# Performance work log

Measured on AMD Instinct MI355X. Metric: run time of the kernel, lower is better.

Reference implementation:

```python
import jax, jax.numpy as jnp
import numpy as np
from jax import lax

L, H = 16384, 1024
EPS = 1e-5


def _ln(x, w, b):
    m = jnp.mean(x, axis=-1, keepdims=True)
    v = jnp.var(x, axis=-1, keepdims=True)
    return (x - m) * lax.rsqrt(v + EPS) * w + b


def setup_inputs() -> dict:
    key = jax.random.key(0)
    ks = jax.random.split(key, 12)
    s = 0.02
    return {
        "x": jax.random.normal(ks[0], (L, H), dtype=jnp.float32),
        "ln1_w": jnp.ones((H,), jnp.float32),
        "ln1_b": jnp.zeros((H,), jnp.float32),
        "W_in": jax.random.normal(ks[1], (H, H), jnp.float32) * s,
        "b_in": jnp.zeros((H,), jnp.float32),
        "W_gate": jax.random.normal(ks[2], (H, H), jnp.float32) * s,
        "b_gate": jnp.zeros((H,), jnp.float32),
        "W_out": jax.random.normal(ks[3], (H, H), jnp.float32) * s,
        "b_out": jnp.zeros((H,), jnp.float32),
        "state_decay": jnp.zeros((H,), jnp.float32),
        "ln2_w": jnp.ones((H,), jnp.float32),
        "ln2_b": jnp.zeros((H,), jnp.float32),
        "W_ff1": jax.random.normal(ks[4], (H, 2 * H), jnp.float32) * s,
        "b_ff1": jnp.zeros((2 * H,), jnp.float32),
        "W_ff2": jax.random.normal(ks[5], (2 * H, H), jnp.float32) * s,
        "b_ff2": jnp.zeros((H,), jnp.float32),
    }


def reference(x, ln1_w, ln1_b, W_in, b_in, W_gate, b_gate, W_out, b_out,
              state_decay, ln2_w, ln2_b, W_ff1, b_ff1, W_ff2, b_ff2):
    hidden = _ln(x, ln1_w, ln1_b)                       # [L,H]
    u = hidden @ W_in + b_in                            # [L,H]
    gate = jax.nn.sigmoid(hidden @ W_gate + b_gate)     # [L,H]
    decay = jax.nn.sigmoid(state_decay)                 # [H]

    def step(s, u_t):
        s = decay * s + u_t
        return s, s

    z = jnp.zeros((x.shape[1],), x.dtype)
    _, states_f = lax.scan(step, z, u)                  # forward recurrence
    _, states_b = lax.scan(step, z, u, reverse=True)    # backward recurrence
    state_out = 0.5 * (states_f + states_b) * gate

    x = x + state_out @ W_out + b_out
    h = _ln(x, ln2_w, ln2_b)
    x = x + jax.nn.silu(h @ W_ff1 + b_ff1) @ W_ff2 + b_ff2
    return x
```

## Files before the change

kernel.cpp:

```cpp
#include <hip/hip_runtime.h>
#include <hip/hip_bf16.h>
#include <hip/hip_fp16.h>

#define L_SEQ 16384
#define HDIM  1024
#define CH    32
#define NC    (L_SEQ / CH)

typedef _Float16 f16;
typedef _Float16 f16x8 __attribute__((ext_vector_type(8)));
typedef _Float16 f16x4 __attribute__((ext_vector_type(4)));
typedef float    f32x4 __attribute__((ext_vector_type(4)));

#define AS1(p) (const __attribute__((address_space(1))) void*)(p)
#define AS3(p) (__attribute__((address_space(3))) void*)(p)

__global__ __launch_bounds__(256) void wcvt_t(const float* __restrict__ in,
                                              f16* __restrict__ out, int K, int N) {
  __shared__ float tile[32][33];
  int n0 = blockIdx.x * 32, k0 = blockIdx.y * 32;
  int tx = threadIdx.x, ty = threadIdx.y;
#pragma unroll
  for (int i = 0; i < 4; i++) {
    int k = k0 + ty + i * 8;
    tile[ty + i * 8][tx] = in[(size_t)k * N + n0 + tx];
  }
  __syncthreads();
#pragma unroll
  for (int i = 0; i < 4; i++) {
    int n = n0 + ty + i * 8;
    out[(size_t)n * K + k0 + tx] = (f16)tile[tx][ty + i * 8];
  }
}

__global__ __launch_bounds__(256) void ln_k(const float* __restrict__ x,
                                            const float* __restrict__ w,
                                            const float* __restrict__ b,
                                            f16* __restrict__ out,
                                            f16* __restrict__ xcopy) {
  int row = blockIdx.x;
  int t = threadIdx.x;
  const float4* xr = (const float4*)(x + (size_t)row * HDIM);
  float4 v = xr[t];
  float s  = v.x + v.y + v.z + v.w;
  float s2 = v.x * v.x + v.y * v.y + v.z * v.z + v.w * v.w;
#pragma unroll
  for (int off = 32; off > 0; off >>= 1) {
    s  += __shfl_down(s, off);
    s2 += __shfl_down(s2, off);
  }
  __shared__ float red[8];
  int wid = t >> 6, lane = t & 63;
  if (lane == 0) { red[wid] = s; red[4 + wid] = s2; }
  __syncthreads();
  if (t == 0) {
    red[0] = red[0] + red[1] + red[2] + red[3];
    red[4] = red[4] + red[5] + red[6] + red[7];
  }
  __syncthreads();
  float mean = red[0] * (1.0f / HDIM);
  float var  = red[4] * (1.0f / HDIM) - mean * mean;
  float rstd = rsqrtf(var + 1e-5f);
  float4 ww = ((const float4*)w)[t];
  float4 bb = ((const float4*)b)[t];
  f16x4 o;
  o[0] = (f16)((v.x - mean) * rstd * ww.x + bb.x);
  o[1] = (f16)((v.y - mean) * rstd * ww.y + bb.y);
  o[2] = (f16)((v.z - mean) * rstd * ww.z + bb.z);
  o[3] = (f16)((v.w - mean) * rstd * ww.w + bb.w);
  ((f16x4*)(out + (size_t)row * HDIM))[t] = o;
  if (xcopy) {
    f16x4 c;
    c[0] = (f16)v.x; c[1] = (f16)v.y; c[2] = (f16)v.z; c[3] = (f16)v.w;
    ((f16x4*)(xcopy + (size_t)row * HDIM))[t] = c;
  }
}

__global__ __launch_bounds__(128) void ln_k16(const f16* __restrict__ x,
                                              const float* __restrict__ w,
                                              const float* __restrict__ b,
                                              f16* __restrict__ out) {
  int row = blockIdx.x;
  int t = threadIdx.x;
  f16x8 xv = ((const f16x8*)(x + (size_t)row * HDIM))[t];
  float v[8];
  float s = 0.f, s2 = 0.f;
#pragma unroll
  for (int i = 0; i < 8; i++) {
    v[i] = (float)xv[i];
    s += v[i]; s2 += v[i] * v[i];
  }
#pragma unroll
  for (int off = 32; off > 0; off >>= 1) {
    s  += __shfl_down(s, off);
    s2 += __shfl_down(s2, off);
  }
  __shared__ float red[4];
  int wid = t >> 6, lane = t & 63;
  if (lane == 0) { red[wid] = s; red[2 + wid] = s2; }
  __syncthreads();
  float mean = (red[0] + red[1]) * (1.0f / HDIM);
  float var  = (red[2] + red[3]) * (1.0f / HDIM) - mean * mean;
  float rstd = rsqrtf(var + 1e-5f);
  float4 w1 = ((const float4*)w)[2 * t], w2 = ((const float4*)w)[2 * t + 1];
  float4 b1 = ((const float4*)b)[2 * t], b2 = ((const float4*)b)[2 * t + 1];
  float wv[8] = {w1.x, w1.y, w1.z, w1.w, w2.x, w2.y, w2.z, w2.w};
  float bv[8] = {b1.x, b1.y, b1.z, b1.w, b2.x, b2.y, b2.z, b2.w};
  f16x8 o;
#pragma unroll
  for (int i = 0; i < 8; i++) o[i] = (f16)((v[i] - mean) * rstd * wv[i] + bv[i]);
  ((f16x8*)(out + (size_t)row * HDIM))[t] = o;
}

template <int MODE, int RESID, int OUTF16>
__global__ __launch_bounds__(256, 5) void gemm_bt(const f16* __restrict__ A,
                                                  const f16* __restrict__ BT,
                                                  const float* __restrict__ bias,
                                                  const float* __restrict__ bias2,
                                                  const f16* __restrict__ resid,
                                                  void* __restrict__ Cout,
                                                  void* __restrict__ Cout2,
                                                  int M, int N, int K) {
  __shared__ __align__(16) f16 As[2][128 * 32];
  __shared__ __align__(16) f16 Bs[2][128 * 32];
  const int tid  = threadIdx.x;
  const int lane = tid & 63, wid = tid >> 6;
  const int wm = wid >> 1, wn = wid & 1;
  const int quad = lane >> 4, l16 = lane & 15;

  const int nbx = N >> 7, nby = M >> 7;
  const int b = blockIdx.x;
  const int xcd = b & 7;
  const int i = b >> 3;
  const int strips = nby >> 3;
  const int rs = i / nbx, cb = i - rs * nbx;
  const long m0 = (long)(xcd * strips + rs) << 7;
  const long n0 = (long)cb << 7;

  const int srow = wid * 16 + (lane >> 2);
  const int qs = (lane & 3) ^ ((srow >> 1) & 3);
  const f16* gA = A  + (m0 + srow) * K + qs * 8;
  const f16* gB = BT + (n0 + srow) * K + qs * 8;
  const int sdst = wid * 1024;

  f32x4 zero = {0.f, 0.f, 0.f, 0.f};
  f32x4 acc[4][4];
#pragma unroll
  for (int i2 = 0; i2 < 4; i2++)
#pragma unroll
    for (int j = 0; j < 4; j++) acc[i2][j] = zero;

#pragma unroll
  for (int it = 0; it < 2; ++it) {
    __builtin_amdgcn_global_load_lds(AS1(gA + (size_t)(it * 64) * K),
                                     AS3((char*)As[0] + it * 4096 + sdst), 16, 0, 0);
    __builtin_amdgcn_global_load_lds(AS1(gB + (size_t)(it * 64) * K),
                                     AS3((char*)Bs[0] + it * 4096 + sdst), 16, 0, 0);
  }
  __syncthreads();

  const int niter = K >> 5;
  for (int ki = 0; ki < niter; ++ki) {
    const int cur = ki & 1;
    if (ki + 1 < niter) {
      const int nxt = cur ^ 1;
      const int koff = (ki + 1) << 5;
#pragma unroll
      for (int it = 0; it < 2; ++it) {
        __builtin_amdgcn_global_load_lds(AS1(gA + (size_t)(it * 64) * K + koff),
                                         AS3((char*)As[nxt] + it * 4096 + sdst), 16, 0, 0);
        __builtin_amdgcn_global_load_lds(AS1(gB + (size_t)(it * 64) * K + koff),
                                         AS3((char*)Bs[nxt] + it * 4096 + sdst), 16, 0, 0);
      }
    }
    f16x8 af[4], bfr[4];
#pragma unroll
    for (int mi = 0; mi < 4; ++mi) {
      const int ar = wm * 64 + mi * 16 + l16;
      af[mi] = *(const f16x8*)(As[cur] + ar * 32 + ((quad ^ ((ar >> 1) & 3)) << 3));
    }
#pragma unroll
    for (int ni = 0; ni < 4; ++ni) {
      const int br = wn * 64 + ni * 16 + l16;
      bfr[ni] = *(const f16x8*)(Bs[cur] + br * 32 + ((quad ^ ((br >> 1) & 3)) << 3));
    }
#pragma unroll
    for (int mi = 0; mi < 4; ++mi)
#pragma unroll
      for (int ni = 0; ni < 4; ++ni)
        acc[mi][ni] = __builtin_amdgcn_mfma_f32_16x16x32_f16(af[mi], bfr[ni], acc[mi][ni], 0, 0, 0);
    __syncthreads();
  }

#pragma unroll
  for (int mi = 0; mi < 4; ++mi) {
#pragma unroll
    for (int ni = 0; ni < 4; ++ni) {
      const long col = n0 + wn * 64 + ni * 16 + l16;
      float bc;
      if (MODE == 3) bc = (col < HDIM) ? bias[col] : bias2[col - HDIM];
      else           bc = bias[col];
#pragma unroll
      for (int r = 0; r < 4; ++r) {
        const long row = m0 + wm * 64 + mi * 16 + quad * 4 + r;
        float v = acc[mi][ni][r] + bc;
        if (MODE == 2) v = v / (1.f + __expf(-v));
        if (MODE == 3) {
          if (col < HDIM) {
            ((f16*)Cout)[row * HDIM + col] = (f16)v;
          } else {
            float g = 1.f / (1.f + __expf(-v));
            ((f16*)Cout2)[row * HDIM + (col - HDIM)] = (f16)g;
          }
        } else {
          if (RESID) v += (float)resid[row * N + col];
          if (OUTF16) ((f16*)Cout)[row * N + col] = (f16)v;
          else        ((float*)Cout)[row * N + col] = v;
        }
      }
    }
  }
}

__global__ __launch_bounds__(256) void scan_p1(const f16* __restrict__ u,
                                               const float* __restrict__ sdecay,
                                               float* __restrict__ carry_f,
                                               float* __restrict__ carry_b) {
  int tid = blockIdx.x * 256 + threadIdx.x;
  int h = tid & (HDIM - 1);
  int c = tid >> 10;
  float d = 1.f / (1.f + expf(-sdecay[h]));
  const f16* up = u + (size_t)c * CH * HDIM + h;
  float sf = 0.f, sb = 0.f, p = 1.f;
#pragma unroll
  for (int i = 0; i < CH; i++) {
    float uu = (float)up[i * HDIM];
    sf = d * sf + uu;
    sb += p * uu;
    p *= d;
  }
  carry_f[(size_t)c * HDIM + h] = sf;
  carry_b[(size_t)c * HDIM + h] = sb;
}

__global__ __launch_bounds__(256) void scan_p2(const float* __restrict__ sdecay,
                                               const float* __restrict__ carry_f,
                                               const float* __restrict__ carry_b,
                                               float* __restrict__ cin_f,
                                               float* __restrict__ cin_b) {
  int tid = blockIdx.x * 256 + threadIdx.x;
  int h = tid & (HDIM - 1);
  int dir = tid >> 10;
  float d = 1.f / (1.f + expf(-sdecay[h]));
  float dT = powf(d, (float)CH);
  float S = 0.f;
  if (dir == 0) {
#pragma unroll 4
    for (int c = 0; c < NC; c++) {
      cin_f[(size_t)c * HDIM + h] = S;
      S = dT * S + carry_f[(size_t)c * HDIM + h];
    }
  } else {
#pragma unroll 4
    for (int c = NC - 1; c >= 0; c--) {
      cin_b[(size_t)c * HDIM + h] = S;
      S = dT * S + carry_b[(size_t)c * HDIM + h];
    }
  }
}

__global__ __launch_bounds__(256) void scan_p3(const f16* __restrict__ u,
                                               const f16* __restrict__ gate,
                                               const float* __restrict__ sdecay,
                                               const float* __restrict__ cin_f,
                                               const float* __restrict__ cin_b,
                                               f16* __restrict__ state_out) {
  int tid = blockIdx.x * 256 + threadIdx.x;
  int h = tid & (HDIM - 1);
  int c = tid >> 10;
  float d = 1.f / (1.f + expf(-sdecay[h]));
  const f16* up = u    + (size_t)c * CH * HDIM + h;
  const f16* gp = gate + (size_t)c * CH * HDIM + h;
  f16* op = state_out  + (size_t)c * CH * HDIM + h;
  float ur[CH], sf[CH];
#pragma unroll
  for (int i = 0; i < CH; i++) ur[i] = (float)up[i * HDIM];
  float s = cin_f[(size_t)c * HDIM + h];
#pragma unroll
  for (int i = 0; i < CH; i++) { s = d * s + ur[i]; sf[i] = s; }
  s = cin_b[(size_t)c * HDIM + h];
#pragma unroll
  for (int i = CH - 1; i >= 0; i--) {
    s = d * s + ur[i];
    float g = (float)gp[i * HDIM];
    op[i * HDIM] = (f16)(0.5f * (sf[i] + s) * g);
  }
}

extern "C" void kernel_launch(void* const* d_in, const int* in_sizes, int n_in,
                              void* d_out, int out_size, void* d_ws, size_t ws_size,
                              hipStream_t stream) {
  const float* x      = (const float*)d_in[0];
  const float* ln1_w  = (const float*)d_in[1];
  const float* ln1_b  = (const float*)d_in[2];
  const float* W_in   = (const float*)d_in[3];
  const float* b_in   = (const float*)d_in[4];
  const float* W_gate = (const float*)d_in[5];
  const float* b_gate = (const float*)d_in[6];
  const float* W_out  = (const float*)d_in[7];
  const float* b_out  = (const float*)d_in[8];
  const float* sdecay = (const float*)d_in[9];
  const float* ln2_w  = (const float*)d_in[10];
  const float* ln2_b  = (const float*)d_in[11];
  const float* W_ff1  = (const float*)d_in[12];
  const float* b_ff1  = (const float*)d_in[13];
  const float* W_ff2  = (const float*)d_in[14];
  const float* b_ff2  = (const float*)d_in[15];
  float* out = (float*)d_out;

  char* ws = (char*)d_ws;
  const size_t MB32 = 33554432, MB64 = 67108864;
  f16* hidden = (f16*)(ws);
  f16* xh     = (f16*)(ws + MB32);
  f16* u      = (f16*)(ws + 2 * MB32);
  f16* gate   = (f16*)(ws + 3 * MB32);
  f16* x2h    = (f16*)(ws + 4 * MB32);
  f16* ff     = (f16*)(ws + 5 * MB32);
  char* wbase = ws + 5 * MB32 + MB64;
  f16* wt_ug  = (f16*)(wbase);
  f16* wt_out = (f16*)(wbase + 4194304);
  f16* wt_ff1 = (f16*)(wbase + 4194304 + 2097152);
  f16* wt_ff2 = (f16*)(wbase + 2 * 4194304 + 2097152);
  char* cbase = wbase + 3 * 4194304 + 2097152;
  float* carry_f = (float*)(cbase);
  float* carry_b = (float*)(cbase + 2097152);
  float* cin_f   = (float*)(cbase + 2 * 2097152);
  float* cin_b   = (float*)(cbase + 3 * 2097152);
  f16* state_out = hidden;
  f16* h2        = u;

  dim3 tb(32, 8);
  wcvt_t<<<dim3(32, 32), tb, 0, stream>>>(W_in,   wt_ug,                 1024, 1024);
  wcvt_t<<<dim3(32, 32), tb, 0, stream>>>(W_gate, wt_ug + 1024 * 1024,   1024, 1024);
  wcvt_t<<<dim3(32, 32), tb, 0, stream>>>(W_out,  wt_out,                1024, 1024);
  wcvt_t<<<dim3(64, 32), tb, 0, stream>>>(W_ff1,  wt_ff1,                1024, 2048);
  wcvt_t<<<dim3(32, 64), tb, 0, stream>>>(W_ff2,  wt_ff2,                2048, 1024);

  ln_k<<<L_SEQ, 256, 0, stream>>>(x, ln1_w, ln1_b, hidden, xh);

  gemm_bt<3, 0, 1><<<2048, 256, 0, stream>>>(hidden, wt_ug, b_in, b_gate, nullptr,
                                             u, gate, L_SEQ, 2048, 1024);

  scan_p1<<<2048, 256, 0, stream>>>(u, sdecay, carry_f, carry_b);
  scan_p2<<<8, 256, 0, stream>>>(sdecay, carry_f, carry_b, cin_f, cin_b);
  scan_p3<<<2048, 256, 0, stream>>>(u, gate, sdecay, cin_f, cin_b, state_out);

  gemm_bt<0, 1, 1><<<1024, 256, 0, stream>>>(state_out, wt_out, b_out, nullptr, xh,
                                             x2h, nullptr, L_SEQ, 1024, 1024);

  ln_k16<<<L_SEQ, 128, 0, stream>>>(x2h, ln2_w, ln2_b, h2);

  gemm_bt<2, 0, 1><<<2048, 256, 0, stream>>>(h2, wt_ff1, b_ff1, nullptr, nullptr,
                                             ff, nullptr, L_SEQ, 2048, 1024);

  gemm_bt<0, 1, 0><<<1024, 256, 0, stream>>>(ff, wt_ff2, b_ff2, nullptr, x2h,
                                             out, nullptr, L_SEQ, 1024, 2048);
}
```

Measured before the change: 636.1 us.

## Triple-buffer GEMM LDS tiles with prefetch distance two and vmcnt waits

The GEMM mainloop goes from double to triple-buffered LDS staging. Tiles are prefetched two K-steps ahead, and the full __syncthreads at the end of each iteration is replaced by a partial s_waitcnt vmcnt(4) plus one barrier at the top. The aim is to hide global-load latency better and cut barrier stalls. In exchange LDS use rises to 48KB per block, so the occupancy hint drops from 5 to 3 blocks per CU.

```diff
diff --git a/kernel.cpp b/kernel.cpp
--- a/kernel.cpp
+++ b/kernel.cpp
@@ -113,7 +113,7 @@
 }
 
 template <int MODE, int RESID, int OUTF16>
-__global__ __launch_bounds__(256, 5) void gemm_bt(const f16* __restrict__ A,
+__global__ __launch_bounds__(256, 3) void gemm_bt(const f16* __restrict__ A,
                                                   const f16* __restrict__ BT,
                                                   const float* __restrict__ bias,
                                                   const float* __restrict__ bias2,
@@ -121,8 +121,8 @@
                                                   void* __restrict__ Cout,
                                                   void* __restrict__ Cout2,
                                                   int M, int N, int K) {
-  __shared__ __align__(16) f16 As[2][128 * 32];
-  __shared__ __align__(16) f16 Bs[2][128 * 32];
+  __shared__ __align__(16) f16 As[3][128 * 32];
+  __shared__ __align__(16) f16 Bs[3][128 * 32];
   const int tid  = threadIdx.x;
   const int lane = tid & 63, wid = tid >> 6;
   const int wm = wid >> 1, wn = wid & 1;
@@ -151,28 +151,41 @@
     for (int j = 0; j < 4; j++) acc[i2][j] = zero;
 
 #pragma unroll
-  for (int it = 0; it < 2; ++it) {
-    __builtin_amdgcn_global_load_lds(AS1(gA + (size_t)(it * 64) * K),
-                                     AS3((char*)As[0] + it * 4096 + sdst), 16, 0, 0);
-    __builtin_amdgcn_global_load_lds(AS1(gB + (size_t)(it * 64) * K),
-                                     AS3((char*)Bs[0] + it * 4096 + sdst), 16, 0, 0);
-  }
-  __syncthreads();
+  for (int pt = 0; pt < 2; ++pt) {
+    const int koff = pt << 5;
+#pragma unroll
+    for (int it = 0; it < 2; ++it) {
+      __builtin_amdgcn_global_load_lds(AS1(gA + (size_t)(it * 64) * K + koff),
+                                       AS3((char*)As[pt] + it * 4096 + sdst), 16, 0, 0);
+      __builtin_amdgcn_global_load_lds(AS1(gB + (size_t)(it * 64) * K + koff),
+                                       AS3((char*)Bs[pt] + it * 4096 + sdst), 16, 0, 0);
+    }
+  }
 
   const int niter = K >> 5;
+  int cur = 0;
   for (int ki = 0; ki < niter; ++ki) {
-    const int cur = ki & 1;
-    if (ki + 1 < niter) {
-      const int nxt = cur ^ 1;
-      const int koff = (ki + 1) << 5;
+    if (ki < niter - 1) {
+      asm volatile("s_waitcnt vmcnt(4)" ::: "memory");
+    } else {
+      asm volatile("s_waitcnt vmcnt(0)" ::: "memory");
+    }
+    __builtin_amdgcn_sched_barrier(0);
+    __builtin_amdgcn_s_barrier();
+    __builtin_amdgcn_sched_barrier(0);
+
+    if (ki + 2 < niter) {
+      const int nb = (cur >= 1) ? cur - 1 : cur + 2;
+      const int koff = (ki + 2) << 5;
 #pragma unroll
       for (int it = 0; it < 2; ++it) {
         __builtin_amdgcn_global_load_lds(AS1(gA + (size_t)(it * 64) * K + koff),
-                                         AS3((char*)As[nxt] + it * 4096 + sdst), 16, 0, 0);
+                                         AS3((char*)As[nb] + it * 4096 + sdst), 16, 0, 0);
         __builtin_amdgcn_global_load_lds(AS1(gB + (size_t)(it * 64) * K + koff),
-                                         AS3((char*)Bs[nxt] + it * 4096 + sdst), 16, 0, 0);
+                                         AS3((char*)Bs[nb] + it * 4096 + sdst), 16, 0, 0);
       }
     }
+
     f16x8 af[4], bfr[4];
 #pragma unroll
     for (int mi = 0; mi < 4; ++mi) {
@@ -189,7 +202,8 @@
 #pragma unroll
       for (int ni = 0; ni < 4; ++ni)
         acc[mi][ni] = __builtin_amdgcn_mfma_f32_16x16x32_f16(af[mi], bfr[ni], acc[mi][ni], 0, 0, 0);
-    __syncthreads();
+
+    cur = (cur == 2) ? 0 : cur + 1;
   }
 
 #pragma unroll
```

Result: slower. 649.0 us (+2.0%).
